# Kernel tuning notes

Hardware: AMD Instinct MI355X
Metric: run time of the kernel (lower is better)

The kernel has to match this reference:

```python
import jax, jax.numpy as jnp
import numpy as np

TOP_K = 2

def setup_inputs() -> dict:
    key = jax.random.key(0)
    ks = jax.random.split(key, 5)
    B, S, D, E, R, H = 4, 2048, 1024, 8, 128, 4096
    s = 0.02
    return {
        "hidden_states": jax.random.normal(ks[0], (B, S, D), jnp.float32),
        "w_route": jax.random.normal(ks[1], (E, D, R), jnp.float32) * s,
        "w3": jax.random.normal(ks[2], (E, D, H), jnp.float32) * s,
        "wr2h": jax.random.normal(ks[3], (E, R, H), jnp.float32) * s,
        "wh2d": jax.random.normal(ks[4], (E, H, D), jnp.float32) * s,
    }

def reference(hidden_states, w_route, w3, wr2h, wh2d):
    B, S, D = hidden_states.shape
    E = w_route.shape[0]
    x = hidden_states.reshape(-1, D)                      # [N, D]
    N = x.shape[0]
    # per-expert routing activations (also reused as w1_state inside experts)
    acts = jnp.einsum('nd,edr->ner', x, w_route)          # [N, E, R]
    norms = jnp.linalg.norm(acts, axis=-1)                # [N, E] router logits
    probs = jax.nn.softmax(norms.astype(jnp.float32), axis=-1)
    topw, sel = jax.lax.top_k(probs, TOP_K)               # [N, k]
    topw = topw / topw.sum(axis=-1, keepdims=True)
    topw = topw.astype(x.dtype)
    # dense combine weights: routing weight if expert selected, else 0
    combine = jnp.zeros((N, E), x.dtype).at[jnp.arange(N)[:, None], sel].add(topw)
    out = jnp.zeros_like(x)
    for e in range(E):  # fixed small expert count
        h = (x @ w3[e]) * jax.nn.silu(acts[:, e, :] @ wr2h[e])  # [N, H]
        out = out + (h @ wh2d[e]) * combine[:, e:e + 1]
    final = out.reshape(B, S, D)
    # load balancing loss on the router logits (expert_act_norms)
    mask = jax.nn.one_hot(sel, E, dtype=jnp.float32)      # [N, k, E]
    tokens_per_expert = mask.mean(axis=0)                 # [k, E]
    router_prob_per_expert = probs.mean(axis=0)           # [E]
    bl_loss = jnp.sum(tokens_per_expert * router_prob_per_expert[None, :]) * E
    return final, norms, bl_loss
```

## Files before the change

kernel.cpp:

```cpp
#include <hip/hip_runtime.h>


#define DEV static __device__ __forceinline__

typedef float  f32x4  __attribute__((ext_vector_type(4)));
typedef __bf16 bf16x8 __attribute__((ext_vector_type(8)));

#define VMCNT_(n) asm volatile("s_waitcnt vmcnt(" #n ")" ::: "memory")
#define VMCNT(n) VMCNT_(n)

DEV unsigned short f2bf(float f) {
  union { float f; unsigned u; } v; v.f = f;
  unsigned r = v.u + 0x7fffu + ((v.u >> 16) & 1u);
  return (unsigned short)(r >> 16);
}
DEV float bf2f(unsigned short b) {
  union { unsigned u; float f; } v; v.u = ((unsigned)b) << 16;
  return v.f;
}

DEV void gll16(const void* g, void* l) {
  __builtin_amdgcn_global_load_lds(
      (const __attribute__((address_space(1))) unsigned int*)g,
      (__attribute__((address_space(3))) unsigned int*)l, 16, 0, 0);
}

DEV f32x4 mfma16(bf16x8 a, bf16x8 b, f32x4 c) {
  return __builtin_amdgcn_mfma_f32_16x16x32_bf16(a, b, c, 0, 0, 0);
}

DEV int xcd_swz_gen(int bid, int nwg) {
  int x = bid & 7, o = bid >> 3;
  int q = nwg >> 3, r = nwg & 7;
  return (x < r ? x * (q + 1) : r * (q + 1) + (x - r) * q) + o;
}

DEV bf16x8 frag_read(const unsigned short* lds, int row, int kb) {
  int off = row * 128 + ((kb * 2) ^ ((row & 7) << 4));
  return *(const bf16x8*)((const char*)lds + off);
}
DEV void stage_linear(const unsigned short* base, size_t pitch, int k0,
                      unsigned short* lds, int tid) {
  int wq = tid >> 6, lane = tid & 63;
#pragma unroll
  for (int i = 0; i < 4; ++i) {
    int s = wq * 256 + i * 64 + lane;
    int row = s >> 3, b = s & 7;
    int bb = b ^ (row & 7);
    const unsigned short* g = base + (size_t)row * pitch + (size_t)(k0 + bb * 8);
    gll16(g, lds + (size_t)(wq * 256 + i * 64) * 8);
  }
}
DEV void mfma_block(const unsigned short* A, const unsigned short* B,
                    f32x4 (&acc)[4][4], int wm, int wn, int lg, int lc) {
#pragma unroll
  for (int ks = 0; ks < 2; ++ks) {
    int kb = ks * 32 + lg * 8;
    bf16x8 af[4], bff[4];
#pragma unroll
    for (int i = 0; i < 4; ++i) {
      af[i]  = frag_read(A, wm * 64 + i * 16 + lc, kb);
      bff[i] = frag_read(B, wn * 64 + i * 16 + lc, kb);
    }
#pragma unroll
    for (int mf = 0; mf < 4; ++mf)
#pragma unroll
      for (int nf = 0; nf < 4; ++nf)
        acc[mf][nf] = mfma16(af[mf], bff[nf], acc[mf][nf]);
  }
}


__global__ __launch_bounds__(256) void k_cast_x(const float* __restrict__ x,
    unsigned short* __restrict__ xh, unsigned short* __restrict__ xl) {
  int stride = gridDim.x * blockDim.x;
  for (int i = blockIdx.x * blockDim.x + threadIdx.x; i < 8192 * 1024 / 4;
       i += stride) {
    float4 v = ((const float4*)x)[i];
    ushort4 h, l;
    h.x = f2bf(v.x); l.x = f2bf(v.x - bf2f(h.x));
    h.y = f2bf(v.y); l.y = f2bf(v.y - bf2f(h.y));
    h.z = f2bf(v.z); l.z = f2bf(v.z - bf2f(h.z));
    h.w = f2bf(v.w); l.w = f2bf(v.w - bf2f(h.w));
    ((ushort4*)xh)[i] = h;
    ((ushort4*)xl)[i] = l;
  }
}

__global__ void k_zero(int* cnt, float* probsum) {
  int t = threadIdx.x;
  if (t < 16) cnt[t] = 0;
  if (t < 8)  probsum[t] = 0.f;
}

__global__ __launch_bounds__(256) void k_transp(const float* __restrict__ src,
    unsigned short* __restrict__ dst, int K, int N) {
  int ntn = N >> 6;
  int kt = blockIdx.x / ntn, nt = blockIdx.x % ntn;
  int e = blockIdx.y;
  __shared__ float tl[64][65];
  const float* s = src + (size_t)e * K * N;
  unsigned short* d = dst + (size_t)e * N * K;
  int tid = threadIdx.x;
  int c4 = (tid & 15) * 4, rr = tid >> 4;
#pragma unroll
  for (int p = 0; p < 4; ++p) {
    int row = rr + p * 16;
    float4 v = *(const float4*)(s + (size_t)(kt * 64 + row) * N + nt * 64 + c4);
    tl[row][c4] = v.x; tl[row][c4 + 1] = v.y;
    tl[row][c4 + 2] = v.z; tl[row][c4 + 3] = v.w;
  }
  __syncthreads();
#pragma unroll
  for (int p = 0; p < 4; ++p) {
    int n = rr + p * 16;
    ushort4 o;
    o.x = f2bf(tl[c4 + 0][n]); o.y = f2bf(tl[c4 + 1][n]);
    o.z = f2bf(tl[c4 + 2][n]); o.w = f2bf(tl[c4 + 3][n]);
    *(ushort4*)(d + (size_t)(nt * 64 + n) * K + kt * 64 + c4) = o;
  }
}

__global__ __launch_bounds__(256) void k_transp_split(const float* __restrict__ src,
    unsigned short* __restrict__ dh, unsigned short* __restrict__ dl, int K, int N) {
  int ntn = N >> 6;
  int kt = blockIdx.x / ntn, nt = blockIdx.x % ntn;
  int e = blockIdx.y;
  __shared__ float tl[64][65];
  const float* s = src + (size_t)e * K * N;
  size_t dbase = (size_t)e * N * K;
  int tid = threadIdx.x;
  int c4 = (tid & 15) * 4, rr = tid >> 4;
#pragma unroll
  for (int p = 0; p < 4; ++p) {
    int row = rr + p * 16;
    float4 v = *(const float4*)(s + (size_t)(kt * 64 + row) * N + nt * 64 + c4);
    tl[row][c4] = v.x; tl[row][c4 + 1] = v.y;
    tl[row][c4 + 2] = v.z; tl[row][c4 + 3] = v.w;
  }
  __syncthreads();
#pragma unroll
  for (int p = 0; p < 4; ++p) {
    int n = rr + p * 16;
    ushort4 oh, ol;
#pragma unroll
    for (int i = 0; i < 4; ++i) {
      float v = tl[c4 + i][n];
      unsigned short hh = f2bf(v);
      unsigned short ll = f2bf(v - bf2f(hh));
      ((unsigned short*)&oh)[i] = hh;
      ((unsigned short*)&ol)[i] = ll;
    }
    *(ushort4*)(dh + dbase + (size_t)(nt * 64 + n) * K + kt * 64 + c4) = oh;
    *(ushort4*)(dl + dbase + (size_t)(nt * 64 + n) * K + kt * 64 + c4) = ol;
  }
}

__global__ __launch_bounds__(256) void k_route_gemm(
    const unsigned short* __restrict__ xh, const unsigned short* __restrict__ xl,
    const unsigned short* __restrict__ wrh_t, const unsigned short* __restrict__ wrl_t,
    unsigned short* __restrict__ acts, float* __restrict__ norms_out) {
  __shared__ __align__(16) unsigned short Ah[128 * 64], Al[128 * 64];
  __shared__ __align__(16) unsigned short Bh[128 * 64], Bl[128 * 64];
  __shared__ float ssq_s[128][2];
  int tid = threadIdx.x;
  int mt = blockIdx.x, e = blockIdx.y;
  int wq = tid >> 6, lane = tid & 63;
  int wm = wq >> 1, wn = wq & 1, lg = lane >> 4, lc = lane & 15;
  f32x4 acc[4][4] = {};
  const unsigned short* ah_src = xh + (size_t)mt * 128 * 1024;
  const unsigned short* al_src = xl + (size_t)mt * 128 * 1024;
  const unsigned short* bh_src = wrh_t + (size_t)e * 128 * 1024;
  const unsigned short* bl_src = wrl_t + (size_t)e * 128 * 1024;
  for (int kt = 0; kt < 16; ++kt) {
    int k0 = kt * 64;
    stage_linear(ah_src, 1024, k0, Ah, tid);
    stage_linear(al_src, 1024, k0, Al, tid);
    stage_linear(bh_src, 1024, k0, Bh, tid);
    stage_linear(bl_src, 1024, k0, Bl, tid);
    __syncthreads();
#pragma unroll
    for (int ks = 0; ks < 2; ++ks) {
      int kb = ks * 32 + lg * 8;
      bf16x8 ahf[4], alf[4], bhf[4], blf[4];
#pragma unroll
      for (int i = 0; i < 4; ++i) {
        ahf[i] = frag_read(Ah, wm * 64 + i * 16 + lc, kb);
        alf[i] = frag_read(Al, wm * 64 + i * 16 + lc, kb);
        bhf[i] = frag_read(Bh, wn * 64 + i * 16 + lc, kb);
        blf[i] = frag_read(Bl, wn * 64 + i * 16 + lc, kb);
      }
#pragma unroll
      for (int mf = 0; mf < 4; ++mf)
#pragma unroll
        for (int nf = 0; nf < 4; ++nf) {
          acc[mf][nf] = mfma16(ahf[mf], bhf[nf], acc[mf][nf]);
          acc[mf][nf] = mfma16(alf[mf], bhf[nf], acc[mf][nf]);
          acc[mf][nf] = mfma16(ahf[mf], blf[nf], acc[mf][nf]);
        }
    }
    __syncthreads();
  }
  float ssq[4][4];
#pragma unroll
  for (int mf = 0; mf < 4; ++mf)
#pragma unroll
    for (int r = 0; r < 4; ++r) ssq[mf][r] = 0.f;
#pragma unroll
  for (int mf = 0; mf < 4; ++mf)
#pragma unroll
    for (int nf = 0; nf < 4; ++nf)
#pragma unroll
      for (int r = 0; r < 4; ++r) {
        float v = acc[mf][nf][r];
        int row = wm * 64 + mf * 16 + lg * 4 + r;
        int col = wn * 64 + nf * 16 + lc;
        acts[(size_t)(mt * 128 + row) * 1024 + e * 128 + col] = f2bf(v);
        ssq[mf][r] += v * v;
      }
#pragma unroll
  for (int mf = 0; mf < 4; ++mf)
#pragma unroll
    for (int r = 0; r < 4; ++r) {
      float s = ssq[mf][r];
      s += __shfl_xor(s, 1); s += __shfl_xor(s, 2);
      s += __shfl_xor(s, 4); s += __shfl_xor(s, 8);
      if (lc == 0) ssq_s[wm * 64 + mf * 16 + lg * 4 + r][wn] = s;
    }
  __syncthreads();
  if (tid < 128) {
    float s = ssq_s[tid][0] + ssq_s[tid][1];
    norms_out[(size_t)(mt * 128 + tid) * 8 + e] = sqrtf(s);
  }
}

__global__ __launch_bounds__(256) void k_router(const float* __restrict__ norms,
    float* __restrict__ topw, int* __restrict__ sel,
    int* __restrict__ cnt, float* __restrict__ probsum) {
  __shared__ float ps_s[8];
  __shared__ int cnt_s[16];
  int tid = threadIdx.x;
  if (tid < 8)  ps_s[tid] = 0.f;
  if (tid < 16) cnt_s[tid] = 0;
  __syncthreads();
  int n = blockIdx.x * 256 + tid;
  float p[8], mx = -3.4e38f;
#pragma unroll
  for (int e = 0; e < 8; ++e) { p[e] = norms[(size_t)n * 8 + e]; mx = fmaxf(mx, p[e]); }
  float s = 0.f;
#pragma unroll
  for (int e = 0; e < 8; ++e) { p[e] = __expf(p[e] - mx); s += p[e]; }
  float inv = 1.f / s;
  int i1 = 0; float v1 = p[0];
#pragma unroll
  for (int e = 1; e < 8; ++e) if (p[e] > v1) { v1 = p[e]; i1 = e; }
  int i2 = -1; float v2 = -1.f;
#pragma unroll
  for (int e = 0; e < 8; ++e) if (e != i1 && p[e] > v2) { v2 = p[e]; i2 = e; }
  float wsum = v1 + v2;
  topw[n * 2 + 0] = v1 / wsum;
  topw[n * 2 + 1] = v2 / wsum;
  sel[n * 2 + 0] = i1;
  sel[n * 2 + 1] = i2;
  atomicAdd(&cnt_s[i1], 1);
  atomicAdd(&cnt_s[8 + i2], 1);
#pragma unroll
  for (int e = 0; e < 8; ++e) atomicAdd(&ps_s[e], p[e] * inv);
  __syncthreads();
  if (tid < 8)  atomicAdd(&probsum[tid], ps_s[tid]);
  if (tid < 16) atomicAdd(&cnt[tid], cnt_s[tid]);
}

__global__ void k_plan(const int* __restrict__ cnt, const float* __restrict__ probsum,
                       int* __restrict__ offs, int* __restrict__ fill,
                       int4* __restrict__ tilemap, float* __restrict__ bl_out) {
  int4* map256 = tilemap;
  int t = 0;
  for (int k = 0; k < 2; ++k) {
    int pos = 0;
    for (int e = 0; e < 8; ++e) {
      int c = cnt[k * 8 + e];
      offs[k * 8 + e] = pos;
      int ntl = (c + 255) >> 8;
      for (int i = 0; i < ntl; ++i) {
        int rr = c - i * 256; if (rr > 256) rr = 256;
        map256[t] = make_int4(e, k * 8192 + pos + i * 256, rr, 0);
        ++t;
      }
      pos += c;
    }
  }
  for (; t < 80; ++t) map256[t] = make_int4(0, 0, 0, 0);
  for (int i = 0; i < 16; ++i) fill[i] = 0;
  float bl = 0.f;
  for (int e = 0; e < 8; ++e)
    bl += ((float)(cnt[e] + cnt[8 + e]) / 8192.f) * (probsum[e] / 8192.f);
  *bl_out = bl * 8.f;
}

__global__ __launch_bounds__(256) void k_fill(const int* __restrict__ sel,
    const float* __restrict__ topw, const int* __restrict__ offs,
    int* __restrict__ fill, int* __restrict__ list01, float* __restrict__ wlist) {
  int n = blockIdx.x * 256 + threadIdx.x;
#pragma unroll
  for (int k = 0; k < 2; ++k) {
    int e = sel[n * 2 + k];
    int pos = atomicAdd(&fill[k * 8 + e], 1);
    int idx = k * 8192 + offs[k * 8 + e] + pos;
    list01[idx] = n;
    wlist[idx] = topw[n * 2 + k];
  }
}

__global__ __launch_bounds__(512, 2) void k_gemm1(
    const unsigned short* __restrict__ xh, const unsigned short* __restrict__ acts,
    const unsigned short* __restrict__ w3t, const unsigned short* __restrict__ wr2h_t,
    const int* __restrict__ list, const int4* __restrict__ map256, int tile_lo,
    int nt, unsigned short* __restrict__ hbuf) {
  __shared__ __align__(16) unsigned short SA[2][256 * 64];
  __shared__ __align__(16) unsigned short SB[2][128 * 64];
  __shared__ int toks[256];
  int wg = xcd_swz_gen((int)blockIdx.x, nt * 32);
  int tloc = wg >> 5, bn = wg & 31;
  int4 ent = map256[tile_lo + tloc];
  int e = ent.x, posbase = ent.y, rows = ent.z;
  if (rows == 0) return;
  int tid = threadIdx.x;
  if (tid < 256) {
    int rr = tid < rows ? tid : rows - 1;
    toks[tid] = list[posbase + rr];
  }
  __syncthreads();
  int wq = tid >> 6, lane = tid & 63;
  int wm = wq >> 2, wn = wq & 3, lg = lane >> 4, lc = lane & 15;

  int s0 = tid, s1 = tid + 512;
  int r0 = s0 >> 3, c0 = ((s0 & 7) ^ (r0 & 7)) * 8;
  int r1 = s1 >> 3, c1 = ((s1 & 7) ^ (r1 & 7)) * 8;
  const unsigned short* a00 = xh + (size_t)toks[r0] * 1024 + c0;
  const unsigned short* a01 = xh + (size_t)toks[r1] * 1024 + c1;
  const unsigned short* a10 = xh + (size_t)toks[128 + r0] * 1024 + c0;
  const unsigned short* a11 = xh + (size_t)toks[128 + r1] * 1024 + c1;
  ptrdiff_t dA = (acts - xh) + e * 128;
  int rb = tid >> 3, cb = ((tid & 7) ^ (rb & 7)) * 8;
  const unsigned short* b0 = w3t + ((size_t)e * 4096 + bn * 128 + rb) * 1024 + cb;
  const unsigned short* b1 = w3t + ((size_t)e * 4096 + bn * 128 + 64 + rb) * 1024 + cb;
  const unsigned short* q0 = wr2h_t + ((size_t)e * 4096 + bn * 128 + rb) * 128 + cb;
  const unsigned short* q1 = wr2h_t + ((size_t)e * 4096 + bn * 128 + 64 + rb) * 128 + cb;

  auto stA = [&](int kt, int h, int bi) {
    unsigned short* d0 = &SA[bi][(size_t)(h * 1024 + s0) * 8];
    unsigned short* d1 = &SA[bi][(size_t)(h * 1024 + s1) * 8];
    const unsigned short* p0 = h ? a10 : a00;
    const unsigned short* p1 = h ? a11 : a01;
    if (kt < 16) { gll16(p0 + kt * 64, d0); gll16(p1 + kt * 64, d1); }
    else {
      gll16(p0 + dA + (kt - 16) * 64, d0);
      gll16(p1 + dA + (kt - 16) * 64, d1);
    }
  };
  auto stB = [&](int kt, int h, int bi) {
    unsigned short* d = &SB[bi][(size_t)(h * 512 + tid) * 8];
    if (kt < 16) gll16((h ? b1 : b0) + kt * 64, d);
    else         gll16((h ? q1 : q0) + (kt - 16) * 64, d);
  };

  f32x4 acc_a[2][4][2] = {}, acc_g[2][4][2] = {};
  bf16x8 af[4][2], bf[2][2];

#define RA1(BI, QM)                                                          \
  _Pragma("unroll") for (int mf = 0; mf < 4; ++mf)                           \
  _Pragma("unroll") for (int k2 = 0; k2 < 2; ++k2)                           \
    af[mf][k2] = frag_read(SA[BI], wm * 128 + QM * 64 + mf * 16 + lc,        \
                           k2 * 32 + lg * 8);
#define RB1(BI, QN)                                                          \
  _Pragma("unroll") for (int k2 = 0; k2 < 2; ++k2)                           \
    bf[QN][k2] = frag_read(SB[BI], wn * 32 + QN * 16 + lc, k2 * 32 + lg * 8);
#define PH1(ACC, QM, QN)                                                     \
  __builtin_amdgcn_sched_barrier(0);                                         \
  __builtin_amdgcn_s_barrier();                                              \
  asm volatile("s_waitcnt lgkmcnt(0)" ::: "memory");                         \
  __builtin_amdgcn_sched_barrier(0);                                         \
  __builtin_amdgcn_s_setprio(1);                                             \
  _Pragma("unroll") for (int mf = 0; mf < 4; ++mf)                           \
  _Pragma("unroll") for (int k2 = 0; k2 < 2; ++k2)                           \
    ACC[QM][mf][QN] = mfma16(af[mf][k2], bf[QN][k2], ACC[QM][mf][QN]);       \
  __builtin_amdgcn_s_setprio(0);                                             \
  __builtin_amdgcn_sched_barrier(0);                                         \
  __builtin_amdgcn_s_barrier();

  stA(0, 0, 0); stA(0, 1, 0); stB(0, 0, 0); stB(0, 1, 0);
  stB(1, 0, 1); stB(1, 1, 1);
  VMCNT(2);
  __builtin_amdgcn_s_barrier();

  for (int it = 0; it < 8; ++it) {
    int u = 2 * it;
    RA1(0, 0); RB1(0, 0); stA(u + 1, 0, 1);
    PH1(acc_a, 0, 0);
    RB1(0, 1); stA(u + 1, 1, 1);
    PH1(acc_a, 0, 1);
    RA1(0, 1); stB(u + 2, 0, 0);
    PH1(acc_a, 1, 1);
    stB(u + 2, 1, 0);
    VMCNT(2);
    PH1(acc_a, 1, 0);
    RA1(1, 0); RB1(1, 0); stA(u + 2, 0, 0);
    PH1(acc_a, 0, 0);
    RB1(1, 1); stA(u + 2, 1, 0);
    PH1(acc_a, 0, 1);
    RA1(1, 1); stB(u + 3, 0, 1);
    PH1(acc_a, 1, 1);
    stB(u + 3, 1, 1);
    VMCNT(2);
    PH1(acc_a, 1, 0);
  }
  {
    RA1(0, 0); RB1(0, 0); stA(17, 0, 1);
    PH1(acc_g, 0, 0);
    RB1(0, 1); stA(17, 1, 1);
    PH1(acc_g, 0, 1);
    RA1(0, 1);
    PH1(acc_g, 1, 1);
    VMCNT(0);
    PH1(acc_g, 1, 0);
    RA1(1, 0); RB1(1, 0);
    PH1(acc_g, 0, 0);
    RB1(1, 1);
    PH1(acc_g, 0, 1);
    RA1(1, 1);
    PH1(acc_g, 1, 1);
    PH1(acc_g, 1, 0);
  }
#undef RA1
#undef RB1
#undef PH1

  size_t hrow0 = (size_t)tloc * 256;
#pragma unroll
  for (int qm = 0; qm < 2; ++qm)
#pragma unroll
    for (int mf = 0; mf < 4; ++mf)
#pragma unroll
      for (int qn = 0; qn < 2; ++qn)
#pragma unroll
        for (int r = 0; r < 4; ++r) {
          int row = wm * 128 + qm * 64 + mf * 16 + lg * 4 + r;
          if (row < rows) {
            int col = wn * 32 + qn * 16 + lc;
            float sv = acc_g[qm][mf][qn][r];
            float hv = acc_a[qm][mf][qn][r] * (sv / (1.f + __expf(-sv)));
            hbuf[(hrow0 + row) * 4096 + (size_t)bn * 128 + col] = f2bf(hv);
          }
        }
}

__global__ __launch_bounds__(512, 2) void k_gemm2(
    const unsigned short* __restrict__ hbuf, const unsigned short* __restrict__ wh2dt,
    const int* __restrict__ list, const float* __restrict__ wlist,
    const int4* __restrict__ map256, int tile_lo, int nt,
    float* __restrict__ out) {
  __shared__ __align__(16) unsigned short SA[2][256 * 64];
  __shared__ __align__(16) unsigned short SB[2][256 * 64];
  __shared__ int toks[256];
  __shared__ float wr_s[256];
  int wg = xcd_swz_gen((int)blockIdx.x, nt * 8);
  int tloc = wg >> 3, bn = (wg >> 1) & 3, ks = wg & 1;
  int4 ent = map256[tile_lo + tloc];
  int e = ent.x, posbase = ent.y, rows = ent.z;
  if (rows == 0) return;
  int tid = threadIdx.x;
  if (tid < 256) {
    int rr = tid < rows ? tid : rows - 1;
    toks[tid] = list[posbase + rr];
    wr_s[tid] = wlist[posbase + rr];
  }
  __syncthreads();
  int wq = tid >> 6, lane = tid & 63;
  int wm = wq >> 2, wn = wq & 3, lg = lane >> 4, lc = lane & 15;
  int kbase = ks * 2048;

  int s0 = tid, s1 = tid + 512;
  int r0 = s0 >> 3, c0 = ((s0 & 7) ^ (r0 & 7)) * 8;
  int r1 = s1 >> 3, c1 = ((s1 & 7) ^ (r1 & 7)) * 8;
  const unsigned short* a0 = hbuf + ((size_t)tloc * 256 + r0) * 4096 + kbase + c0;
  const unsigned short* a1 = hbuf + ((size_t)tloc * 256 + r1) * 4096 + kbase + c1;
  const unsigned short* b0 =
      wh2dt + ((size_t)e * 1024 + bn * 256 + r0) * 4096 + kbase + c0;
  const unsigned short* b1 =
      wh2dt + ((size_t)e * 1024 + bn * 256 + r1) * 4096 + kbase + c1;

  auto stA = [&](int kt, int h, int bi) {
    size_t ho = (size_t)h * 128 * 4096;
    gll16(a0 + ho + kt * 64, &SA[bi][(size_t)(h * 1024 + s0) * 8]);
    gll16(a1 + ho + kt * 64, &SA[bi][(size_t)(h * 1024 + s1) * 8]);
  };
  auto stB = [&](int kt, int h, int bi) {
    size_t ho = (size_t)h * 128 * 4096;
    gll16(b0 + ho + kt * 64, &SB[bi][(size_t)(h * 1024 + s0) * 8]);
    gll16(b1 + ho + kt * 64, &SB[bi][(size_t)(h * 1024 + s1) * 8]);
  };

  f32x4 acc[2][4][2][2] = {};
  bf16x8 af[4][2], bf[2][2][2];

#define RA(BI, QM)                                                           \
  _Pragma("unroll") for (int mf = 0; mf < 4; ++mf)                           \
  _Pragma("unroll") for (int k2 = 0; k2 < 2; ++k2)                           \
    af[mf][k2] = frag_read(SA[BI], wm * 128 + QM * 64 + mf * 16 + lc,        \
                           k2 * 32 + lg * 8);
#define RB(BI, QN)                                                           \
  _Pragma("unroll") for (int nf = 0; nf < 2; ++nf)                           \
  _Pragma("unroll") for (int k2 = 0; k2 < 2; ++k2)                           \
    bf[QN][nf][k2] = frag_read(SB[BI], wn * 64 + QN * 32 + nf * 16 + lc,     \
                               k2 * 32 + lg * 8);
#define PH_MMA(QM, QN)                                                       \
  __builtin_amdgcn_sched_barrier(0);                                         \
  __builtin_amdgcn_s_barrier();                                              \
  asm volatile("s_waitcnt lgkmcnt(0)" ::: "memory");                         \
  __builtin_amdgcn_sched_barrier(0);                                         \
  __builtin_amdgcn_s_setprio(1);                                             \
  _Pragma("unroll") for (int mf = 0; mf < 4; ++mf)                           \
  _Pragma("unroll") for (int nf = 0; nf < 2; ++nf)                           \
  _Pragma("unroll") for (int k2 = 0; k2 < 2; ++k2)                           \
    acc[QM][mf][QN][nf] =                                                    \
        mfma16(af[mf][k2], bf[QN][nf][k2], acc[QM][mf][QN][nf]);             \
  __builtin_amdgcn_s_setprio(0);                                             \
  __builtin_amdgcn_sched_barrier(0);                                         \
  __builtin_amdgcn_s_barrier();

  stA(0, 0, 0); stA(0, 1, 0); stB(0, 0, 0); stB(0, 1, 0);
  stB(1, 0, 1); stB(1, 1, 1);
  VMCNT(4);
  __builtin_amdgcn_s_barrier();

  for (int it = 0; it < 15; ++it) {
    int u = 2 * it;
    RA(0, 0); RB(0, 0); stA(u + 1, 0, 1);
    PH_MMA(0, 0);
    RB(0, 1); stA(u + 1, 1, 1);
    PH_MMA(0, 1);
    RA(0, 1); stB(u + 2, 0, 0);
    PH_MMA(1, 1);
    stB(u + 2, 1, 0);
    VMCNT(4);
    PH_MMA(1, 0);
    RA(1, 0); RB(1, 0); stA(u + 2, 0, 0);
    PH_MMA(0, 0);
    RB(1, 1); stA(u + 2, 1, 0);
    PH_MMA(0, 1);
    RA(1, 1); stB(u + 3, 0, 1);
    PH_MMA(1, 1);
    stB(u + 3, 1, 1);
    VMCNT(4);
    PH_MMA(1, 0);
  }
  {
    RA(0, 0); RB(0, 0); stA(31, 0, 1);
    PH_MMA(0, 0);
    RB(0, 1); stA(31, 1, 1);
    PH_MMA(0, 1);
    RA(0, 1);
    PH_MMA(1, 1);
    VMCNT(0);
    PH_MMA(1, 0);
    RA(1, 0); RB(1, 0);
    PH_MMA(0, 0);
    RB(1, 1);
    PH_MMA(0, 1);
    RA(1, 1);
    PH_MMA(1, 1);
    PH_MMA(1, 0);
  }
#undef RA
#undef RB
#undef PH_MMA

#pragma unroll
  for (int qm = 0; qm < 2; ++qm)
#pragma unroll
    for (int mf = 0; mf < 4; ++mf)
#pragma unroll
      for (int qn = 0; qn < 2; ++qn)
#pragma unroll
        for (int nf = 0; nf < 2; ++nf)
#pragma unroll
          for (int r = 0; r < 4; ++r) {
            int row = wm * 128 + qm * 64 + mf * 16 + lg * 4 + r;
            if (row < rows) {
              int col = wn * 64 + qn * 32 + nf * 16 + lc;
              float v = acc[qm][mf][qn][nf][r] * wr_s[row];
              atomicAdd(out + (size_t)toks[row] * 1024 + bn * 256 + col, v);
            }
          }
}


extern "C" void kernel_launch(void* const* d_in, const int* in_sizes, int n_in,
                              void* d_out, int out_size, void* d_ws, size_t ws_size,
                              hipStream_t stream) {
  (void)in_sizes; (void)n_in; (void)out_size;
  const float* x      = (const float*)d_in[0];
  const float* wroute = (const float*)d_in[1];
  const float* w3     = (const float*)d_in[2];
  const float* wr2h   = (const float*)d_in[3];
  const float* wh2d   = (const float*)d_in[4];
  float* out = (float*)d_out;

  char* ws = (char*)d_ws;
  size_t off = 0;
  auto carve = [&](size_t bytes) -> void* {
    void* p = ws + off; off += (bytes + 255) & ~(size_t)255; return p;
  };
  unsigned short* xh     = (unsigned short*)carve((size_t)8192 * 1024 * 2);
  unsigned short* xl     = (unsigned short*)carve((size_t)8192 * 1024 * 2);
  unsigned short* wrh_t  = (unsigned short*)carve((size_t)8 * 128 * 1024 * 2);
  unsigned short* wrl_t  = (unsigned short*)carve((size_t)8 * 128 * 1024 * 2);
  unsigned short* w3t    = (unsigned short*)carve((size_t)8 * 4096 * 1024 * 2);
  unsigned short* wr2h_t = (unsigned short*)carve((size_t)8 * 4096 * 128 * 2);
  unsigned short* wh2dt  = (unsigned short*)carve((size_t)8 * 1024 * 4096 * 2);
  unsigned short* acts   = (unsigned short*)carve((size_t)8192 * 1024 * 2);
  int*   list01 = (int*)carve(2 * 8192 * 4);
  float* wlist  = (float*)carve(2 * 8192 * 4);
  int*   sel    = (int*)carve(8192 * 2 * 4);
  float* topw   = (float*)carve(8192 * 2 * 4);
  int*   ctr    = (int*)carve(8192);
  int* cnt = ctr; int* fill = ctr + 16; int* offs = ctr + 32;
  float* probsum = (float*)(ctr + 48);
  int4* tilemap = (int4*)(ctr + 64);

  size_t avail = ws_size > off ? ws_size - off : 0;
  int tpc = 0;
  const int cands[4] = {160, 80, 40, 20};
  for (int i = 0; i < 4; ++i) {
    if ((size_t)cands[i] * 128 * 4096 * 2 <= avail) { tpc = cands[i]; break; }
  }
  if (!tpc) return;
  unsigned short* hbuf = (unsigned short*)(ws + off);

  float* norms_out = out + 8388608;
  float* bl_out    = out + 8454144;

  hipMemsetAsync(out, 0, (size_t)8388608 * 4, stream);
  k_cast_x<<<2048, 256, 0, stream>>>(x, xh, xl);
  k_zero<<<1, 64, 0, stream>>>(cnt, probsum);
  k_transp<<<dim3(16 * 64, 8), 256, 0, stream>>>(w3, w3t, 1024, 4096);
  k_transp<<<dim3(64 * 16, 8), 256, 0, stream>>>(wh2d, wh2dt, 4096, 1024);
  k_transp<<<dim3(2 * 64, 8), 256, 0, stream>>>(wr2h, wr2h_t, 128, 4096);
  k_transp_split<<<dim3(16 * 2, 8), 256, 0, stream>>>(wroute, wrh_t, wrl_t, 1024, 128);
  k_route_gemm<<<dim3(64, 8), 256, 0, stream>>>(xh, xl, wrh_t, wrl_t, acts, norms_out);
  k_router<<<32, 256, 0, stream>>>(norms_out, topw, sel, cnt, probsum);
  k_plan<<<1, 1, 0, stream>>>(cnt, probsum, offs, fill, tilemap, bl_out);
  k_fill<<<32, 256, 0, stream>>>(sel, topw, offs, fill, list01, wlist);

  int nchunk = (160 + tpc - 1) / tpc;
  for (int c = 0; c < nchunk; ++c) {
    int tile_lo = c * tpc;
    int nt = 160 - tile_lo < tpc ? 160 - tile_lo : tpc;
    k_gemm1<<<(nt / 2) * 32, 512, 0, stream>>>(
        xh, acts, w3t, wr2h_t, list01, tilemap, tile_lo / 2, nt / 2, hbuf);
    k_gemm2<<<(nt / 2) * 8, 512, 0, stream>>>(
        hbuf, wh2dt, list01, wlist, tilemap, tile_lo / 2, nt / 2, out);
  }
}
```

Baseline: 784.2 us.

## Triple-buffer gemm1 LDS tiles and simplify the k-loop to two phases

Moves the first expert GEMM from double-buffered to triple-buffered shared memory for the A (token) and B (weight) tiles, prefetching two k-steps ahead with combined A+B loads. Each k-step now runs two larger MFMA phases instead of four, which halves the barriers per step. The cost is higher LDS use (about 144KB per block), which likely conflicts with launch_bounds(512,2) occupancy and may drop residency to one block per CU. The pipeline depth and vmcnt accounting are also reworked.

```diff
diff --git a/kernel.cpp b/kernel.cpp
--- a/kernel.cpp
+++ b/kernel.cpp
@@ -317,8 +317,8 @@
     const unsigned short* __restrict__ w3t, const unsigned short* __restrict__ wr2h_t,
     const int* __restrict__ list, const int4* __restrict__ map256, int tile_lo,
     int nt, unsigned short* __restrict__ hbuf) {
-  __shared__ __align__(16) unsigned short SA[2][256 * 64];
-  __shared__ __align__(16) unsigned short SB[2][128 * 64];
+  __shared__ __align__(16) unsigned short SA[3][256 * 64];
+  __shared__ __align__(16) unsigned short SB[3][128 * 64];
   __shared__ int toks[256];
   int wg = xcd_swz_gen((int)blockIdx.x, nt * 32);
   int tloc = wg >> 5, bn = wg & 31;
@@ -348,21 +348,21 @@
   const unsigned short* q0 = wr2h_t + ((size_t)e * 4096 + bn * 128 + rb) * 128 + cb;
   const unsigned short* q1 = wr2h_t + ((size_t)e * 4096 + bn * 128 + 64 + rb) * 128 + cb;
 
-  auto stA = [&](int kt, int h, int bi) {
-    unsigned short* d0 = &SA[bi][(size_t)(h * 1024 + s0) * 8];
-    unsigned short* d1 = &SA[bi][(size_t)(h * 1024 + s1) * 8];
-    const unsigned short* p0 = h ? a10 : a00;
-    const unsigned short* p1 = h ? a11 : a01;
-    if (kt < 16) { gll16(p0 + kt * 64, d0); gll16(p1 + kt * 64, d1); }
-    else {
-      gll16(p0 + dA + (kt - 16) * 64, d0);
-      gll16(p1 + dA + (kt - 16) * 64, d1);
+  auto stH = [&](int kt, int h, int bi) {
+    unsigned short* dA0 = &SA[bi][(size_t)(h * 1024 + s0) * 8];
+    unsigned short* dA1 = &SA[bi][(size_t)(h * 1024 + s1) * 8];
+    unsigned short* dB  = &SB[bi][(size_t)(h * 512 + tid) * 8];
+    const unsigned short* pA0 = h ? a10 : a00;
+    const unsigned short* pA1 = h ? a11 : a01;
+    if (kt < 16) {
+      gll16(pA0 + kt * 64, dA0);
+      gll16(pA1 + kt * 64, dA1);
+      gll16((h ? b1 : b0) + kt * 64, dB);
+    } else {
+      gll16(pA0 + dA + (kt - 16) * 64, dA0);
+      gll16(pA1 + dA + (kt - 16) * 64, dA1);
+      gll16((h ? q1 : q0) + (kt - 16) * 64, dB);
     }
-  };
-  auto stB = [&](int kt, int h, int bi) {
-    unsigned short* d = &SB[bi][(size_t)(h * 512 + tid) * 8];
-    if (kt < 16) gll16((h ? b1 : b0) + kt * 64, d);
-    else         gll16((h ? q1 : q0) + (kt - 16) * 64, d);
   };
 
   f32x4 acc_a[2][4][2] = {}, acc_g[2][4][2] = {};
@@ -373,64 +373,51 @@
   _Pragma("unroll") for (int k2 = 0; k2 < 2; ++k2)                           \
     af[mf][k2] = frag_read(SA[BI], wm * 128 + QM * 64 + mf * 16 + lc,        \
                            k2 * 32 + lg * 8);
-#define RB1(BI, QN)                                                          \
+#define RB1(BI)                                                              \
+  _Pragma("unroll") for (int qn = 0; qn < 2; ++qn)                           \
   _Pragma("unroll") for (int k2 = 0; k2 < 2; ++k2)                           \
-    bf[QN][k2] = frag_read(SB[BI], wn * 32 + QN * 16 + lc, k2 * 32 + lg * 8);
-#define PH1(ACC, QM, QN)                                                     \
+    bf[qn][k2] = frag_read(SB[BI], wn * 32 + qn * 16 + lc, k2 * 32 + lg * 8);
+#define PH1(ACC, QM)                                                         \
   __builtin_amdgcn_sched_barrier(0);                                         \
   __builtin_amdgcn_s_barrier();                                              \
   asm volatile("s_waitcnt lgkmcnt(0)" ::: "memory");                         \
   __builtin_amdgcn_sched_barrier(0);                                         \
   __builtin_amdgcn_s_setprio(1);                                             \
   _Pragma("unroll") for (int mf = 0; mf < 4; ++mf)                           \
+  _Pragma("unroll") for (int qn = 0; qn < 2; ++qn)                           \
   _Pragma("unroll") for (int k2 = 0; k2 < 2; ++k2)                           \
-    ACC[QM][mf][QN] = mfma16(af[mf][k2], bf[QN][k2], ACC[QM][mf][QN]);       \
+    ACC[QM][mf][qn] = mfma16(af[mf][k2], bf[qn][k2], ACC[QM][mf][qn]);       \
   __builtin_amdgcn_s_setprio(0);                                             \
   __builtin_amdgcn_sched_barrier(0);                                         \
   __builtin_amdgcn_s_barrier();
 
-  stA(0, 0, 0); stA(0, 1, 0); stB(0, 0, 0); stB(0, 1, 0);
-  stB(1, 0, 1); stB(1, 1, 1);
-  VMCNT(2);
+  stH(0, 0, 0); stH(0, 1, 0);
+  stH(1, 0, 1); stH(1, 1, 1);
+  VMCNT(6);
   __builtin_amdgcn_s_barrier();
 
-  for (int it = 0; it < 8; ++it) {
-    int u = 2 * it;
-    RA1(0, 0); RB1(0, 0); stA(u + 1, 0, 1);
-    PH1(acc_a, 0, 0);
-    RB1(0, 1); stA(u + 1, 1, 1);
-    PH1(acc_a, 0, 1);
-    RA1(0, 1); stB(u + 2, 0, 0);
-    PH1(acc_a, 1, 1);
-    stB(u + 2, 1, 0);
-    VMCNT(2);
-    PH1(acc_a, 1, 0);
-    RA1(1, 0); RB1(1, 0); stA(u + 2, 0, 0);
-    PH1(acc_a, 0, 0);
-    RB1(1, 1); stA(u + 2, 1, 0);
-    PH1(acc_a, 0, 1);
-    RA1(1, 1); stB(u + 3, 0, 1);
-    PH1(acc_a, 1, 1);
-    stB(u + 3, 1, 1);
-    VMCNT(2);
-    PH1(acc_a, 1, 0);
+  for (int t = 0; t < 16; ++t) {
+    int bufi = t % 3, dsti = (t + 2) % 3;
+    stH(t + 2, 0, dsti);
+    RA1(bufi, 0); RB1(bufi);
+    PH1(acc_a, 0);
+    stH(t + 2, 1, dsti);
+    VMCNT(6);
+    RA1(bufi, 1);
+    PH1(acc_a, 1);
   }
   {
-    RA1(0, 0); RB1(0, 0); stA(17, 0, 1);
-    PH1(acc_g, 0, 0);
-    RB1(0, 1); stA(17, 1, 1);
-    PH1(acc_g, 0, 1);
-    RA1(0, 1);
-    PH1(acc_g, 1, 1);
+    RA1(1, 0); RB1(1);
+    PH1(acc_g, 0);
     VMCNT(0);
-    PH1(acc_g, 1, 0);
-    RA1(1, 0); RB1(1, 0);
-    PH1(acc_g, 0, 0);
-    RB1(1, 1);
-    PH1(acc_g, 0, 1);
     RA1(1, 1);
-    PH1(acc_g, 1, 1);
-    PH1(acc_g, 1, 0);
+    PH1(acc_g, 1);
+  }
+  {
+    RA1(2, 0); RB1(2);
+    PH1(acc_g, 0);
+    RA1(2, 1);
+    PH1(acc_g, 1);
   }
 #undef RA1
 #undef RB1
```

Result: slower. 890.2 us (+13.5%).
